# Performance work log

Measured on AMD Instinct MI355X. Metric: run time of the kernel, lower is better.

## Reference

```python
import jax, jax.numpy as jnp
import numpy as np

B, T, DIM, H = 2, 2048, 1024, 16
HD = DIM // H  # head_dim = 64
ROPE_BASE = 10000.0


def setup_inputs() -> dict:
    key = jax.random.key(0)
    k1, k2, k3, k4 = jax.random.split(key, 4)
    s = 1.0 / np.sqrt(DIM)
    return {
        "x": jax.random.normal(k1, (B, T, DIM), dtype=jnp.float32),
        "Wqkv": jax.random.normal(k2, (DIM, 3 * DIM), dtype=jnp.float32) * s,
        "Wout": jax.random.normal(k3, (DIM, DIM), dtype=jnp.float32) * s,
        "bout": jax.random.normal(k4, (DIM,), dtype=jnp.float32) * 0.01,
    }


def _rotate_half(x):
    # interleaved rotation: (x0,x1,x2,x3,...) -> (-x1,x0,-x3,x2,...)
    x1 = x[..., ::2]
    x2 = x[..., 1::2]
    return jnp.stack((-x2, x1), axis=-1).reshape(x.shape)


def _rope_cos_sin(seq_len, dtype):
    inv_freq = 1.0 / (ROPE_BASE ** (jnp.arange(0, HD, 2, dtype=jnp.float32) / HD))
    t = jnp.arange(seq_len, dtype=jnp.float32)
    freqs = t[:, None] * inv_freq[None, :]          # [T, HD/2]
    emb = jnp.concatenate((freqs, freqs), axis=-1)  # [T, HD] (cat layout, as in source)
    return jnp.cos(emb).astype(dtype), jnp.sin(emb).astype(dtype)


def reference(x, Wqkv, Wout, bout):
    b, t, _ = x.shape
    qkv = x @ Wqkv                                  # [B, T, 3*DIM]
    q, k, v = jnp.split(qkv, 3, axis=-1)
    # b t (h d) -> b h t d
    reshape = lambda z: z.reshape(b, t, H, HD).transpose(0, 2, 1, 3)
    q, k, v = reshape(q), reshape(k), reshape(v)
    cos, sin = _rope_cos_sin(t, x.dtype)            # [T, HD]
    q = q * cos + _rotate_half(q) * sin
    k = k * cos + _rotate_half(k) * sin
    scale = HD ** -0.5
    scores = jnp.einsum("bhqd,bhkd->bhqk", q, k) * scale
    attn = jax.nn.softmax(scores, axis=-1)
    out = jnp.einsum("bhqk,bhkd->bhqd", attn, v)    # [B, H, T, HD]
    out = out.transpose(0, 2, 1, 3).reshape(b, t, DIM)
    return out @ Wout + bout
```

## Files before the change

kernel.cpp:

```cpp
#include <hip/hip_runtime.h>
#include <math.h>


typedef unsigned short u16;
typedef __attribute__((ext_vector_type(8))) short short8;
typedef __attribute__((ext_vector_type(4))) short short4v;
typedef __attribute__((ext_vector_type(4))) float f32x4;
typedef __attribute__((ext_vector_type(16))) float f32x16;

#define T_SEQ 2048

__device__ __forceinline__ float b2f(u16 u) {
    union { unsigned int i; float f; } x; x.i = ((unsigned int)u) << 16; return x.f;
}
__device__ __forceinline__ u16 f2b(float f) {
    union { float f; unsigned int i; } x; x.f = f;
    return (u16)((x.i + 0x7FFFu + ((x.i >> 16) & 1u)) >> 16);
}
__device__ __forceinline__ void gl_lds16(const u16* g, u16* l) {
    __builtin_amdgcn_global_load_lds(
        (const __attribute__((address_space(1))) unsigned int*)g,
        (__attribute__((address_space(3))) unsigned int*)l, 16, 0, 0);
}
__device__ __forceinline__ short4v pack4(float a, float b, float c, float d) {
    union { float f; unsigned int u; } xa, xb, xc, xd;
    xa.f = a; xb.f = b; xc.f = c; xd.f = d;
    union { unsigned int u2[2]; short4v s; } r;
    r.u2[0] = (xa.u >> 16) | (xb.u & 0xffff0000u);
    r.u2[1] = (xc.u >> 16) | (xd.u & 0xffff0000u);
    return r.s;
}

__global__ __launch_bounds__(256) void setup_kernel(
    const float* __restrict__ x, const float* __restrict__ Wqkv,
    const float* __restrict__ Wout, u16* __restrict__ xb,
    u16* __restrict__ WqkvT, u16* __restrict__ WoutT,
    float* __restrict__ costab, float* __restrict__ sintab)
{
    const int bid = blockIdx.x;
    const int tid = threadIdx.x;

    if (bid < 4096) {
        int i = (bid * 256 + tid) * 4;
        float4 v = *(const float4*)(x + i);
        ushort4 w;
        w.x = f2b(v.x); w.y = f2b(v.y); w.z = f2b(v.z); w.w = f2b(v.w);
        *(ushort4*)(xb + i) = w;
        return;
    }
    if (bid < 8192) {
        const float* in; u16* out; int R, Cn, bx, by;
        if (bid < 7168) { in = Wqkv; out = WqkvT; R = 1024; Cn = 3072;
                          int id = bid - 4096; bx = id % 96; by = id / 96; }
        else            { in = Wout; out = WoutT; R = 1024; Cn = 1024;
                          int id = bid - 7168; bx = id & 31; by = id >> 5; }
        __shared__ u16 tile[32][33];
        const int tx = tid & 31, ty = tid >> 5;
        const int r0 = by * 32, c0 = bx * 32;
#pragma unroll
        for (int rr = ty; rr < 32; rr += 8)
            tile[tx][rr] = f2b(in[(size_t)(r0 + rr) * Cn + c0 + tx]);
        __syncthreads();
#pragma unroll
        for (int rr = ty; rr < 32; rr += 8)
            out[(size_t)(c0 + rr) * R + r0 + tx] = tile[rr][tx];
        return;
    }
    {
        int idx = (bid - 8192) * 256 + tid;
        int t = idx >> 6, d = idx & 63;
        const float nl32 = -0.28782313662425576f;
        float f = __expf((float)(d & 31) * nl32);
        float s, c;
        __sincosf((float)t * f, &s, &c);
        costab[idx] = c; sintab[idx] = s;
    }
}

template<int OBF>
__global__ __launch_bounds__(256) void gemm_bt_mfma(
    const u16* __restrict__ A, const u16* __restrict__ Bt,
    void* __restrict__ Cv, const float* __restrict__ bias,
    int M, int N, int K)
{
    __shared__ u16 As[128 * 32];
    __shared__ u16 Bs[128 * 32];

    const int tid = threadIdx.x;
    const int wave = tid >> 6, lane = tid & 63;
    const int col = lane & 15, quad = lane >> 4;
    const int wm = (wave & 1) * 64, wn = (wave >> 1) * 64;
    const int m0 = blockIdx.y * 128, n0 = blockIdx.x * 128;

    f32x4 acc[4][4];
#pragma unroll
    for (int i = 0; i < 4; ++i)
#pragma unroll
        for (int j = 0; j < 4; ++j) acc[i][j] = f32x4{0.f, 0.f, 0.f, 0.f};

    const int c1 = tid, c2 = tid + 256;
    const u16* a1 = A + (size_t)(m0 + (c1 >> 2)) * K + (c1 & 3) * 8;
    const u16* a2 = A + (size_t)(m0 + (c2 >> 2)) * K + (c2 & 3) * 8;
    const u16* b1 = Bt + (size_t)(n0 + (c1 >> 2)) * K + (c1 & 3) * 8;
    const u16* b2 = Bt + (size_t)(n0 + (c2 >> 2)) * K + (c2 & 3) * 8;
    u16* la1 = As + c1 * 8; u16* la2 = As + c2 * 8;
    u16* lb1 = Bs + c1 * 8; u16* lb2 = Bs + c2 * 8;

    for (int k0 = 0; k0 < K; k0 += 32) {
        __syncthreads();
        gl_lds16(a1 + k0, la1);
        gl_lds16(a2 + k0, la2);
        gl_lds16(b1 + k0, lb1);
        gl_lds16(b2 + k0, lb2);
        __syncthreads();

        short8 af[4], bfr[4];
#pragma unroll
        for (int i = 0; i < 4; ++i) {
            af[i]  = *(const short8*)&As[(wm + i * 16 + col) * 32 + quad * 8];
            bfr[i] = *(const short8*)&Bs[(wn + i * 16 + col) * 32 + quad * 8];
        }
#pragma unroll
        for (int i = 0; i < 4; ++i)
#pragma unroll
            for (int j = 0; j < 4; ++j)
                acc[i][j] = __builtin_amdgcn_mfma_f32_16x16x32_bf16(
                    af[i], bfr[j], acc[i][j], 0, 0, 0);
    }

#pragma unroll
    for (int j = 0; j < 4; ++j) {
        int n = n0 + wn + j * 16 + col;
        float bv = bias ? bias[n] : 0.f;
#pragma unroll
        for (int i = 0; i < 4; ++i) {
            int mbase = m0 + wm + i * 16 + quad * 4;
#pragma unroll
            for (int r = 0; r < 4; ++r) {
                if (OBF) ((u16*)Cv)[(size_t)(mbase + r) * N + n] = f2b(acc[i][j][r] + bv);
                else     ((float*)Cv)[(size_t)(mbase + r) * N + n] = acc[i][j][r] + bv;
            }
        }
    }
}

__global__ __launch_bounds__(256) void prep_kernel(
    const u16* __restrict__ qkvb, const float* __restrict__ costab,
    const float* __restrict__ sintab, u16* __restrict__ Qb,
    u16* __restrict__ Kb, u16* __restrict__ Vtb)
{
    __shared__ u16 Vls[64][72];

    const int tid = threadIdx.x;
    const int bh = blockIdx.y;
    const int t0 = blockIdx.x * 64;
    const int b = bh >> 4, h = bh & 15;
    const int t_loc = tid >> 2;
    const int d0 = (tid & 3) * 16;

    const int t = t0 + t_loc;
    const u16* qp = qkvb + ((size_t)(b * T_SEQ + t)) * 3072 + h * 64 + d0;

    float ct[16], st[16];
    {
        const float* cp = costab + (size_t)t * 64 + d0;
        const float* sp = sintab + (size_t)t * 64 + d0;
#pragma unroll
        for (int j = 0; j < 16; j += 4) {
            *(float4*)&ct[j] = *(const float4*)(cp + j);
            *(float4*)&st[j] = *(const float4*)(sp + j);
        }
    }

#pragma unroll
    for (int part = 0; part < 2; ++part) {
        const float sc = part ? 1.f : 0.125f;
        const u16* src = qp + part * 1024;
        u16* dst = (part ? Kb : Qb) + ((size_t)(bh * T_SEQ + t)) * 64 + d0;
        short8 v0 = *(const short8*)(src);
        short8 v1 = *(const short8*)(src + 8);
        float f[16];
#pragma unroll
        for (int j = 0; j < 8; ++j) { f[j] = b2f((u16)v0[j]); f[8 + j] = b2f((u16)v1[j]); }
        u16 o[16];
#pragma unroll
        for (int i = 0; i < 8; ++i) {
            float e = f[2 * i], od = f[2 * i + 1];
            o[2 * i]     = f2b((e * ct[2 * i]      - od * st[2 * i]) * sc);
            o[2 * i + 1] = f2b((od * ct[2 * i + 1] + e  * st[2 * i + 1]) * sc);
        }
        *(short8*)(dst)     = *(short8*)&o[0];
        *(short8*)(dst + 8) = *(short8*)&o[8];
    }

    {
        const u16* src = qp + 2048;
        *(short8*)&Vls[t_loc][d0]     = *(const short8*)(src);
        *(short8*)&Vls[t_loc][d0 + 8] = *(const short8*)(src + 8);
    }
    __syncthreads();
    {
        const int d_loc = tid >> 2;
        const int tc = tid & 3;
        u16 o[16];
#pragma unroll
        for (int j = 0; j < 16; ++j) o[j] = Vls[tc * 16 + j][d_loc];
        u16* dst = Vtb + ((size_t)(bh * 64 + d_loc)) * T_SEQ + t0 + tc * 16;
        *(short8*)(dst)     = *(short8*)&o[0];
        *(short8*)(dst + 8) = *(short8*)&o[8];
    }
}

__global__ __launch_bounds__(256) void attn32_kernel(
    const u16* __restrict__ Qb, const u16* __restrict__ Kb,
    const u16* __restrict__ Vtb, float* __restrict__ po, float* __restrict__ pl)
{
    __shared__ u16 Kfrag[256 * 8];
    __shared__ u16 Vfrag[256 * 8];

    const int tid = threadIdx.x;
    const int wave = tid >> 6, lane = tid & 63;
    const int qcol = lane & 31;
    const int hi = lane >> 5;

    const int bid = blockIdx.x;
    const int bh = bid >> 5;
    const int seg = (bid >> 4) & 1;
    const int qblk = bid & 15;
    const int qrow0 = qblk * 128 + wave * 32;

    short8 qa[4];
    {
        const u16* qp = Qb + ((size_t)(bh * T_SEQ + qrow0 + qcol)) * 64 + hi * 8;
#pragma unroll
        for (int c = 0; c < 4; ++c) qa[c] = *(const short8*)(qp + c * 16);
    }

    short4v ones4;
#pragma unroll
    for (int j = 0; j < 4; ++j) ones4[j] = (short)0x3F80;

    f32x16 O0, O1, L;
#pragma unroll
    for (int i = 0; i < 16; ++i) { O0[i] = 0.f; O1[i] = 0.f; L[i] = 0.f; }

    const u16* kg_ptr = Kb + ((size_t)bh * T_SEQ + qcol) * 64 + wave * 16 + hi * 8;
    u16* kl = Kfrag + tid * 8;
    const int vd = tid >> 2;
    const int vkg = (tid & 3) ^ ((vd >> 1) & 3);
    const u16* vg_ptr = Vtb + ((size_t)(bh * 64 + vd)) * T_SEQ + vkg * 8;
    u16* vl = Vfrag + tid * 8;

    const int vsw = (qcol >> 1) & 3;
    const int vbase = qcol * 32 + hi * 4;

    const int kt0 = seg * 32;
    for (int kt = kt0; kt < kt0 + 32; ++kt) {
        __syncthreads();
        gl_lds16(kg_ptr + (size_t)kt * 2048, kl);
        gl_lds16(vg_ptr + kt * 32, vl);
        __syncthreads();

        short8 kf[4];
#pragma unroll
        for (int f = 0; f < 4; ++f)
            kf[f] = *(const short8*)(Kfrag + (f * 64 + lane) * 8);

        f32x16 sT;
#pragma unroll
        for (int i = 0; i < 16; ++i) sT[i] = 0.f;
#pragma unroll
        for (int c = 0; c < 4; ++c)
            sT = __builtin_amdgcn_mfma_f32_32x32x16_bf16(kf[c], qa[c], sT, 0, 0, 0);

        short4v pb[4];
#pragma unroll
        for (int g = 0; g < 4; ++g)
            pb[g] = pack4(__expf(sT[4 * g + 0]), __expf(sT[4 * g + 1]),
                          __expf(sT[4 * g + 2]), __expf(sT[4 * g + 3]));

#pragma unroll
        for (int g = 0; g < 4; ++g) {
            const int gs = (g ^ vsw) * 8;
            short4v va0 = *(const short4v*)(Vfrag + vbase + gs);
            short4v va1 = *(const short4v*)(Vfrag + 1024 + vbase + gs);
            O0 = __builtin_amdgcn_mfma_f32_32x32x8bf16_1k(va0, pb[g], O0, 0, 0, 0);
            O1 = __builtin_amdgcn_mfma_f32_32x32x8bf16_1k(va1, pb[g], O1, 0, 0, 0);
            L  = __builtin_amdgcn_mfma_f32_32x32x8bf16_1k(ones4, pb[g], L, 0, 0, 0);
        }
    }

    const size_t prow = ((size_t)(seg * 32 + bh)) * T_SEQ + qrow0 + qcol;
    float* op = po + prow * 64;
#pragma unroll
    for (int g2 = 0; g2 < 4; ++g2) {
        int dd = g2 * 8 + hi * 4;
        *(float4*)(op + dd)      = make_float4(O0[4 * g2 + 0], O0[4 * g2 + 1],
                                               O0[4 * g2 + 2], O0[4 * g2 + 3]);
        *(float4*)(op + 32 + dd) = make_float4(O1[4 * g2 + 0], O1[4 * g2 + 1],
                                               O1[4 * g2 + 2], O1[4 * g2 + 3]);
    }
    if (hi == 0) pl[prow] = L[0];
}

__global__ __launch_bounds__(256) void attn_combine_kernel(
    const float* __restrict__ po, const float* __restrict__ pl,
    u16* __restrict__ aob)
{
    const int idx = blockIdx.x * 256 + (int)threadIdx.x;
    const int row = idx >> 4;
    const int d4 = idx & 15;

    float4 o0 = *(const float4*)(po + (size_t)row * 64 + d4 * 4);
    float4 o1 = *(const float4*)(po + ((size_t)row + 65536) * 64 + d4 * 4);
    float L = pl[row] + pl[row + 65536];
    float inv = 1.f / L;

    const int bh = row >> 11, t = row & 2047;
    const int b = bh >> 4, h = bh & 15;
    ushort4 w;
    w.x = f2b((o0.x + o1.x) * inv);
    w.y = f2b((o0.y + o1.y) * inv);
    w.z = f2b((o0.z + o1.z) * inv);
    w.w = f2b((o0.w + o1.w) * inv);
    *(ushort4*)(aob + ((size_t)(b * T_SEQ + t)) * 1024 + h * 64 + d4 * 4) = w;
}

extern "C" void kernel_launch(void* const* d_in, const int* in_sizes, int n_in,
                              void* d_out, int out_size, void* d_ws, size_t ws_size,
                              hipStream_t stream)
{
    const float* x    = (const float*)d_in[0];
    const float* Wqkv = (const float*)d_in[1];
    const float* Wout = (const float*)d_in[2];
    const float* bout = (const float*)d_in[3];
    float* out = (float*)d_out;

    char* w = (char*)d_ws;
    u16* qkvb    = (u16*)(w);
    u16* xb      = (u16*)(w + 25165824);
    u16* WqkvT   = (u16*)(w + 33554432);
    u16* WoutT   = (u16*)(w + 39845888);
    u16* aob     = (u16*)(w + 41943040);
    u16* Qb      = (u16*)(w + 50331648);
    u16* Kb      = (u16*)(w + 58720256);
    u16* Vtb     = (u16*)(w + 67108864);
    float* ctab  = (float*)(w + 75497472);
    float* stab  = (float*)(w + 76021760);
    float* po    = (float*)(w);
    float* pl    = (float*)(w + 33554432);

    dim3 blk(256);
    setup_kernel<<<dim3(8704), blk, 0, stream>>>(x, Wqkv, Wout, xb, WqkvT, WoutT, ctab, stab);
    gemm_bt_mfma<1><<<dim3(24, 32), blk, 0, stream>>>(xb, WqkvT, qkvb, nullptr, 4096, 3072, 1024);
    prep_kernel<<<dim3(32, 32), blk, 0, stream>>>(qkvb, ctab, stab, Qb, Kb, Vtb);
    attn32_kernel<<<dim3(1024), blk, 0, stream>>>(Qb, Kb, Vtb, po, pl);
    attn_combine_kernel<<<dim3(4096), blk, 0, stream>>>(po, pl, aob);
    gemm_bt_mfma<0><<<dim3(8, 32), blk, 0, stream>>>(aob, WoutT, out, bout, 4096, 1024, 1024);
}
```

Baseline: 223.6 us.

## Pre-tile V into MFMA fragment order and double-buffer K/V LDS loads

```diff
diff --git a/kernel.cpp b/kernel.cpp
--- a/kernel.cpp
+++ b/kernel.cpp
@@ -147,7 +147,7 @@
 __global__ __launch_bounds__(256) void prep_kernel(
     const u16* __restrict__ qkvb, const float* __restrict__ costab,
     const float* __restrict__ sintab, u16* __restrict__ Qb,
-    u16* __restrict__ Kb, u16* __restrict__ Vtb)
+    u16* __restrict__ Kb, u16* __restrict__ Vimg)
 {
     __shared__ u16 Vls[64][72];
 
@@ -200,23 +200,33 @@
     }
     __syncthreads();
     {
-        const int d_loc = tid >> 2;
-        const int tc = tid & 3;
-        u16 o[16];
-#pragma unroll
-        for (int j = 0; j < 16; ++j) o[j] = Vls[tc * 16 + j][d_loc];
-        u16* dst = Vtb + ((size_t)(bh * 64 + d_loc)) * T_SEQ + t0 + tc * 16;
-        *(short8*)(dst)     = *(short8*)&o[0];
-        *(short8*)(dst + 8) = *(short8*)&o[8];
+        const int dt    = tid >> 7;
+        const int g     = (tid >> 5) & 3;
+        const int hi2   = (tid >> 4) & 1;
+        const int dpair = tid & 15;
+        const int kl0 = g * 8 + hi2 * 4;
+        const int d0v = dt * 32 + 2 * dpair;
+        const int kt_base = blockIdx.x * 2;
+#pragma unroll
+        for (int ktl = 0; ktl < 2; ++ktl) {
+            u16 o[8];
+#pragma unroll
+            for (int j = 0; j < 4; ++j) {
+                o[j]     = Vls[ktl * 32 + kl0 + j][d0v];
+                o[4 + j] = Vls[ktl * 32 + kl0 + j][d0v + 1];
+            }
+            u16* dst = Vimg + ((size_t)(bh * 64 + kt_base + ktl)) * 2048 + tid * 8;
+            *(short8*)dst = *(short8*)&o[0];
+        }
     }
 }
 
 __global__ __launch_bounds__(256) void attn32_kernel(
     const u16* __restrict__ Qb, const u16* __restrict__ Kb,
-    const u16* __restrict__ Vtb, float* __restrict__ po, float* __restrict__ pl)
-{
-    __shared__ u16 Kfrag[256 * 8];
-    __shared__ u16 Vfrag[256 * 8];
+    const u16* __restrict__ Vimg, float* __restrict__ po, float* __restrict__ pl)
+{
+    __shared__ u16 Kbuf[2][2048];
+    __shared__ u16 Vbuf[2][2048];
 
     const int tid = threadIdx.x;
     const int wave = tid >> 6, lane = tid & 63;
@@ -245,30 +255,28 @@
     for (int i = 0; i < 16; ++i) { O0[i] = 0.f; O1[i] = 0.f; L[i] = 0.f; }
 
     const u16* kg_ptr = Kb + ((size_t)bh * T_SEQ + qcol) * 64 + wave * 16 + hi * 8;
-    u16* kl = Kfrag + tid * 8;
-    const int vd = tid >> 2;
-    const int vkg = (tid & 3) ^ ((vd >> 1) & 3);
-    const u16* vg_ptr = Vtb + ((size_t)(bh * 64 + vd)) * T_SEQ + vkg * 8;
-    u16* vl = Vfrag + tid * 8;
-
-    const int vsw = (qcol >> 1) & 3;
-    const int vbase = qcol * 32 + hi * 4;
+    const u16* vg_ptr = Vimg + ((size_t)bh * 64) * 2048 + tid * 8;
 
     const int kt0 = seg * 32;
-    for (int kt = kt0; kt < kt0 + 32; ++kt) {
+    gl_lds16(kg_ptr + (size_t)kt0 * 2048, &Kbuf[0][tid * 8]);
+    gl_lds16(vg_ptr + (size_t)kt0 * 2048, &Vbuf[0][tid * 8]);
+
+    for (int i = 0; i < 32; ++i) {
+        const int buf = i & 1;
         __syncthreads();
-        gl_lds16(kg_ptr + (size_t)kt * 2048, kl);
-        gl_lds16(vg_ptr + kt * 32, vl);
-        __syncthreads();
+        if (i < 31) {
+            gl_lds16(kg_ptr + (size_t)(kt0 + i + 1) * 2048, &Kbuf[buf ^ 1][tid * 8]);
+            gl_lds16(vg_ptr + (size_t)(kt0 + i + 1) * 2048, &Vbuf[buf ^ 1][tid * 8]);
+        }
 
         short8 kf[4];
 #pragma unroll
         for (int f = 0; f < 4; ++f)
-            kf[f] = *(const short8*)(Kfrag + (f * 64 + lane) * 8);
+            kf[f] = *(const short8*)&Kbuf[buf][(f * 64 + lane) * 8];
 
         f32x16 sT;
 #pragma unroll
-        for (int i = 0; i < 16; ++i) sT[i] = 0.f;
+        for (int ii = 0; ii < 16; ++ii) sT[ii] = 0.f;
 #pragma unroll
         for (int c = 0; c < 4; ++c)
             sT = __builtin_amdgcn_mfma_f32_32x32x16_bf16(kf[c], qa[c], sT, 0, 0, 0);
@@ -281,9 +289,8 @@
 
 #pragma unroll
         for (int g = 0; g < 4; ++g) {
-            const int gs = (g ^ vsw) * 8;
-            short4v va0 = *(const short4v*)(Vfrag + vbase + gs);
-            short4v va1 = *(const short4v*)(Vfrag + 1024 + vbase + gs);
+            short4v va0 = *(const short4v*)&Vbuf[buf][g * 256 + lane * 4];
+            short4v va1 = *(const short4v*)&Vbuf[buf][1024 + g * 256 + lane * 4];
             O0 = __builtin_amdgcn_mfma_f32_32x32x8bf16_1k(va0, pb[g], O0, 0, 0, 0);
             O1 = __builtin_amdgcn_mfma_f32_32x32x8bf16_1k(va1, pb[g], O1, 0, 0, 0);
             L  = __builtin_amdgcn_mfma_f32_32x32x8bf16_1k(ones4, pb[g], L, 0, 0, 0);
@@ -344,7 +351,7 @@
     u16* aob     = (u16*)(w + 41943040);
     u16* Qb      = (u16*)(w + 50331648);
     u16* Kb      = (u16*)(w + 58720256);
-    u16* Vtb     = (u16*)(w + 67108864);
+    u16* Vimg    = (u16*)(w + 67108864);
     float* ctab  = (float*)(w + 75497472);
     float* stab  = (float*)(w + 76021760);
     float* po    = (float*)(w);
@@ -353,8 +360,8 @@
     dim3 blk(256);
     setup_kernel<<<dim3(8704), blk, 0, stream>>>(x, Wqkv, Wout, xb, WqkvT, WoutT, ctab, stab);
     gemm_bt_mfma<1><<<dim3(24, 32), blk, 0, stream>>>(xb, WqkvT, qkvb, nullptr, 4096, 3072, 1024);
-    prep_kernel<<<dim3(32, 32), blk, 0, stream>>>(qkvb, ctab, stab, Qb, Kb, Vtb);
-    attn32_kernel<<<dim3(1024), blk, 0, stream>>>(Qb, Kb, Vtb, po, pl);
+    prep_kernel<<<dim3(32, 32), blk, 0, stream>>>(qkvb, ctab, stab, Qb, Kb, Vimg);
+    attn32_kernel<<<dim3(1024), blk, 0, stream>>>(Qb, Kb, Vimg, po, pl);
     attn_combine_kernel<<<dim3(4096), blk, 0, stream>>>(po, pl, aob);
     gemm_bt_mfma<0><<<dim3(8, 32), blk, 0, stream>>>(aob, WoutT, out, bout, 4096, 1024, 1024);
 }
```

Result: slower. 237.3 us (+6.1%).
